# Optimization experiments

Measured on AMD Instinct MI355X. Metric: run time of the kernel, lower is better.

## Reference

```python
import jax, jax.numpy as jnp
import numpy as np

B, C, H, W = 2, 512, 48, 48
HEADS = 8
REDUCTION = 4
DPH = max(C // REDUCTION // HEADS, 1)   # 16
TOTAL = DPH * HEADS                      # 128
EPS_NORM = 1e-12
EPS_BN = 1e-5


def setup_inputs() -> dict:
    key = jax.random.key(0)
    ks = jax.random.split(key, 6)
    x = jax.random.normal(ks[0], (B, C, H, W), dtype=jnp.float32)
    # 1x1 convs stored as [out_ch, in_ch] matrices
    w_qkv = jax.random.normal(ks[1], (3 * TOTAL, C), dtype=jnp.float32) * (1.0 / np.sqrt(C))
    w_out = jax.random.normal(ks[2], (C, TOTAL), dtype=jnp.float32) * (1.0 / np.sqrt(TOTAL))
    temperature = jnp.ones((HEADS, 1, 1), dtype=jnp.float32)
    bn_gamma = jnp.ones((C,), dtype=jnp.float32)
    bn_beta = jnp.zeros((C,), dtype=jnp.float32)
    return {"x": x, "w_qkv": w_qkv, "temperature": temperature,
            "w_out": w_out, "bn_gamma": bn_gamma, "bn_beta": bn_beta}


def _l2norm(t):
    # F.normalize(t, dim=-1): t / max(||t||_2, eps)
    n = jnp.sqrt(jnp.sum(t * t, axis=-1, keepdims=True))
    return t / jnp.maximum(n, EPS_NORM)


def reference(x, w_qkv, temperature, w_out, bn_gamma, bn_beta):
    b, c, h, w = x.shape
    n = h * w
    # qkv 1x1 conv: [b, 3*TOTAL, h, w]
    qkv = jnp.einsum('bchw,oc->bohw', x, w_qkv)
    q, k, v = jnp.split(qkv, 3, axis=1)
    # [b, heads, dph, n] -> [b, heads, n, dph]
    def heads_tokens(t):
        return t.reshape(b, HEADS, DPH, n).transpose(0, 1, 3, 2)
    q = _l2norm(heads_tokens(q))
    k = _l2norm(heads_tokens(k))
    v = heads_tokens(v)
    # [b, heads, n, n]
    attn = jnp.einsum('bhnd,bhmd->bhnm', q, k) * temperature[None]
    attn = jax.nn.softmax(attn, axis=-1)
    out = jnp.einsum('bhnm,bhmd->bhnd', attn, v)          # [b, heads, n, dph]
    out = out.transpose(0, 1, 3, 2).reshape(b, TOTAL, h, w)
    # project_out: 1x1 conv then BatchNorm2d (training-mode batch stats)
    out = jnp.einsum('bthw,ct->bchw', out, w_out)
    mean = jnp.mean(out, axis=(0, 2, 3))
    var = jnp.mean((out - mean[None, :, None, None]) ** 2, axis=(0, 2, 3))
    out = (out - mean[None, :, None, None]) * jax.lax.rsqrt(var + EPS_BN)[None, :, None, None]
    out = out * bn_gamma[None, :, None, None] + bn_beta[None, :, None, None]
    return out
```

## Files before the change

### kernel.cpp

```cpp
#include <hip/hip_runtime.h>

#define NB 2
#define CC 512
#define NN 2304
#define NH 8
#define DD 16
#define TT 128
#define O3 384

typedef __attribute__((ext_vector_type(4))) float f32x4;
typedef __attribute__((ext_vector_type(8))) __bf16 bf16x8;
typedef __attribute__((ext_vector_type(4))) __bf16 bf16x4;
typedef __attribute__((ext_vector_type(4))) _Float16 f16x4;
typedef __attribute__((ext_vector_type(2))) __fp16 hf16x2;

union hf2pair {
    hf16x2 h[2];
    f16x4  v;
};

#define OFF_Q  0u
#define OFF_K  1179648u
#define OFF_VT 2359296u
#define OFF_AO 3538944u

__global__ __launch_bounds__(256) void k1_qkv(
    const float* __restrict__ x, const float* __restrict__ wqkv,
    _Float16* __restrict__ Q, _Float16* __restrict__ K, _Float16* __restrict__ VT)
{
    __shared__ __bf16 As[64][520];
    int ob = blockIdx.x, nt = blockIdx.y, b = blockIdx.z;
    int tid = threadIdx.x;
    int lane = tid & 63, wave = tid >> 6;
    int quad = lane >> 4, col = lane & 15;
    int n0 = nt * 64;
    int o0 = ob * 64;

    {
        int cb = tid >> 4;
        int nq = (tid & 15) * 4;
#pragma unroll
        for (int it = 0; it < 32; ++it) {
            int c = it * 16 + cb;
            f32x4 v = *(const f32x4*)(x + ((size_t)b * CC + c) * NN + n0 + nq);
            As[nq + 0][c] = (__bf16)v[0];
            As[nq + 1][c] = (__bf16)v[1];
            As[nq + 2][c] = (__bf16)v[2];
            As[nq + 3][c] = (__bf16)v[3];
        }
    }
    __syncthreads();

    f32x4 acc0 = {0.f,0.f,0.f,0.f}, acc1 = {0.f,0.f,0.f,0.f};
    f32x4 acc2 = {0.f,0.f,0.f,0.f}, acc3 = {0.f,0.f,0.f,0.f};

    int nrow = wave * 16 + col;
    const float* w0p = wqkv + (size_t)(o0 + col) * CC + quad * 8;
    const float* w1p = w0p + 16 * CC;
    const float* w2p = w0p + 32 * CC;
    const float* w3p = w0p + 48 * CC;

    f32x4 cw0a = *(const f32x4*)(w0p),     cw0b = *(const f32x4*)(w0p + 4);
    f32x4 cw1a = *(const f32x4*)(w1p),     cw1b = *(const f32x4*)(w1p + 4);
    f32x4 cw2a = *(const f32x4*)(w2p),     cw2b = *(const f32x4*)(w2p + 4);
    f32x4 cw3a = *(const f32x4*)(w3p),     cw3b = *(const f32x4*)(w3p + 4);

#pragma unroll
    for (int ks = 0; ks < 16; ks++) {
        f32x4 nw0a, nw0b, nw1a, nw1b, nw2a, nw2b, nw3a, nw3b;
        if (ks < 15) {
            nw0a = *(const f32x4*)(w0p + (ks + 1) * 32);
            nw0b = *(const f32x4*)(w0p + (ks + 1) * 32 + 4);
            nw1a = *(const f32x4*)(w1p + (ks + 1) * 32);
            nw1b = *(const f32x4*)(w1p + (ks + 1) * 32 + 4);
            nw2a = *(const f32x4*)(w2p + (ks + 1) * 32);
            nw2b = *(const f32x4*)(w2p + (ks + 1) * 32 + 4);
            nw3a = *(const f32x4*)(w3p + (ks + 1) * 32);
            nw3b = *(const f32x4*)(w3p + (ks + 1) * 32 + 4);
        }
        bf16x8 a = *(const bf16x8*)(&As[nrow][quad * 8 + ks * 32]);
        bf16x8 wf0, wf1, wf2, wf3;
#pragma unroll
        for (int j = 0; j < 4; j++) {
            wf0[j] = (__bf16)cw0a[j]; wf0[j + 4] = (__bf16)cw0b[j];
            wf1[j] = (__bf16)cw1a[j]; wf1[j + 4] = (__bf16)cw1b[j];
            wf2[j] = (__bf16)cw2a[j]; wf2[j + 4] = (__bf16)cw2b[j];
            wf3[j] = (__bf16)cw3a[j]; wf3[j + 4] = (__bf16)cw3b[j];
        }
        acc0 = __builtin_amdgcn_mfma_f32_16x16x32_bf16(a, wf0, acc0, 0, 0, 0);
        acc1 = __builtin_amdgcn_mfma_f32_16x16x32_bf16(a, wf1, acc1, 0, 0, 0);
        acc2 = __builtin_amdgcn_mfma_f32_16x16x32_bf16(a, wf2, acc2, 0, 0, 0);
        acc3 = __builtin_amdgcn_mfma_f32_16x16x32_bf16(a, wf3, acc3, 0, 0, 0);
        cw0a = nw0a; cw0b = nw0b; cw1a = nw1a; cw1b = nw1b;
        cw2a = nw2a; cw2b = nw2b; cw3a = nw3a; cw3b = nw3b;
    }

#pragma unroll
    for (int s = 0; s < 4; s++) {
        int oc = o0 + s * 16 + col;
        int d = oc & 15, h = (oc >> 4) & 7, kind = oc >> 7;
        f32x4 v = (s == 0) ? acc0 : (s == 1) ? acc1 : (s == 2) ? acc2 : acc3;
        if (kind < 2) {
            float ss0 = v[0] * v[0], ss1 = v[1] * v[1], ss2 = v[2] * v[2], ss3 = v[3] * v[3];
#pragma unroll
            for (int m = 1; m < 16; m <<= 1) {
                ss0 += __shfl_xor(ss0, m);
                ss1 += __shfl_xor(ss1, m);
                ss2 += __shfl_xor(ss2, m);
                ss3 += __shfl_xor(ss3, m);
            }
            v[0] *= 1.0f / fmaxf(sqrtf(ss0), 1e-12f);
            v[1] *= 1.0f / fmaxf(sqrtf(ss1), 1e-12f);
            v[2] *= 1.0f / fmaxf(sqrtf(ss2), 1e-12f);
            v[3] *= 1.0f / fmaxf(sqrtf(ss3), 1e-12f);
            _Float16* dst = (kind == 0 ? Q : K) + (size_t)(b * NH + h) * NN * DD;
#pragma unroll
            for (int r = 0; r < 4; r++) {
                int n = n0 + wave * 16 + quad * 4 + r;
                dst[(size_t)n * DD + d] = (_Float16)v[r];
            }
        } else {
            f16x4 pk;
#pragma unroll
            for (int r = 0; r < 4; r++) pk[r] = (_Float16)v[r];
            int n = n0 + wave * 16 + quad * 4;
            *(f16x4*)(VT + (size_t)((b * NH + h) * DD + d) * NN + n) = pk;
        }
    }
}

__global__ __launch_bounds__(512) void k2_attn(
    const _Float16* __restrict__ Q, const _Float16* __restrict__ K,
    const _Float16* __restrict__ VT, const float* __restrict__ temp,
    __bf16* __restrict__ AO)
{
    __shared__ float Osh[8][16][64];
    __shared__ float Lsh[8][64];

    int qt = blockIdx.x, bh = blockIdx.y;
    int lane = threadIdx.x & 63, wave = threadIdx.x >> 6;
    int quad = lane >> 4, col = lane & 15;
    int kbase = wave * 288;
    int qbase = qt * 64;

    const _Float16* Qb = Q + (size_t)bh * NN * DD;
    float tl2 = temp[bh & 7] * 1.4426950408889634f;
    _Float16 tl2h = (_Float16)tl2;

    f16x4 qf0 = *(const f16x4*)(Qb + (size_t)(qbase +  0 + col) * DD + quad * 4);
    f16x4 qf1 = *(const f16x4*)(Qb + (size_t)(qbase + 16 + col) * DD + quad * 4);
    f16x4 qf2 = *(const f16x4*)(Qb + (size_t)(qbase + 32 + col) * DD + quad * 4);
    f16x4 qf3 = *(const f16x4*)(Qb + (size_t)(qbase + 48 + col) * DD + quad * 4);
#pragma unroll
    for (int j = 0; j < 4; j++) {
        qf0[j] *= tl2h; qf1[j] *= tl2h; qf2[j] *= tl2h; qf3[j] *= tl2h;
    }
    const f16x4 onesf = {(_Float16)1.f, (_Float16)1.f, (_Float16)1.f, (_Float16)1.f};

    f32x4 oa0 = {0.f,0.f,0.f,0.f}, oa1 = {0.f,0.f,0.f,0.f};
    f32x4 oa2 = {0.f,0.f,0.f,0.f}, oa3 = {0.f,0.f,0.f,0.f};
    f32x4 lc0 = {0.f,0.f,0.f,0.f}, lc1 = {0.f,0.f,0.f,0.f};
    f32x4 lc2 = {0.f,0.f,0.f,0.f}, lc3 = {0.f,0.f,0.f,0.f};
    const f32x4 zc = {0.f,0.f,0.f,0.f};

    const _Float16* kp = K + (size_t)bh * NN * DD + (size_t)(kbase + col) * DD + quad * 4;
    const _Float16* vp = VT + (size_t)bh * DD * NN + (size_t)col * NN + kbase + quad * 4;

    f16x4 kfa = *(const f16x4*)(kp);
    f16x4 kfb = *(const f16x4*)(kp + 16 * DD);
    f16x4 vfa = *(const f16x4*)(vp);
    f16x4 vfb = *(const f16x4*)(vp + 16);

#define K2_CHUNK(KF, VF)                                                        \
    {                                                                           \
        f32x4 s0 = __builtin_amdgcn_mfma_f32_16x16x16f16(KF, qf0, zc, 0, 0, 0); \
        f32x4 s1 = __builtin_amdgcn_mfma_f32_16x16x16f16(KF, qf1, zc, 0, 0, 0); \
        f32x4 s2 = __builtin_amdgcn_mfma_f32_16x16x16f16(KF, qf2, zc, 0, 0, 0); \
        f32x4 s3 = __builtin_amdgcn_mfma_f32_16x16x16f16(KF, qf3, zc, 0, 0, 0); \
        hf2pair u0, u1, u2, u3;                                                 \
        u0.h[0] = __builtin_amdgcn_cvt_pkrtz(__builtin_amdgcn_exp2f(s0[0]),     \
                                             __builtin_amdgcn_exp2f(s0[1]));    \
        u0.h[1] = __builtin_amdgcn_cvt_pkrtz(__builtin_amdgcn_exp2f(s0[2]),     \
                                             __builtin_amdgcn_exp2f(s0[3]));    \
        u1.h[0] = __builtin_amdgcn_cvt_pkrtz(__builtin_amdgcn_exp2f(s1[0]),     \
                                             __builtin_amdgcn_exp2f(s1[1]));    \
        u1.h[1] = __builtin_amdgcn_cvt_pkrtz(__builtin_amdgcn_exp2f(s1[2]),     \
                                             __builtin_amdgcn_exp2f(s1[3]));    \
        u2.h[0] = __builtin_amdgcn_cvt_pkrtz(__builtin_amdgcn_exp2f(s2[0]),     \
                                             __builtin_amdgcn_exp2f(s2[1]));    \
        u2.h[1] = __builtin_amdgcn_cvt_pkrtz(__builtin_amdgcn_exp2f(s2[2]),     \
                                             __builtin_amdgcn_exp2f(s2[3]));    \
        u3.h[0] = __builtin_amdgcn_cvt_pkrtz(__builtin_amdgcn_exp2f(s3[0]),     \
                                             __builtin_amdgcn_exp2f(s3[1]));    \
        u3.h[1] = __builtin_amdgcn_cvt_pkrtz(__builtin_amdgcn_exp2f(s3[2]),     \
                                             __builtin_amdgcn_exp2f(s3[3]));    \
        f16x4 p0 = u0.v, p1 = u1.v, p2 = u2.v, p3 = u3.v;                       \
        lc0 = __builtin_amdgcn_mfma_f32_16x16x16f16(onesf, p0, lc0, 0, 0, 0);   \
        lc1 = __builtin_amdgcn_mfma_f32_16x16x16f16(onesf, p1, lc1, 0, 0, 0);   \
        lc2 = __builtin_amdgcn_mfma_f32_16x16x16f16(onesf, p2, lc2, 0, 0, 0);   \
        lc3 = __builtin_amdgcn_mfma_f32_16x16x16f16(onesf, p3, lc3, 0, 0, 0);   \
        oa0 = __builtin_amdgcn_mfma_f32_16x16x16f16(VF, p0, oa0, 0, 0, 0);      \
        oa1 = __builtin_amdgcn_mfma_f32_16x16x16f16(VF, p1, oa1, 0, 0, 0);      \
        oa2 = __builtin_amdgcn_mfma_f32_16x16x16f16(VF, p2, oa2, 0, 0, 0);      \
        oa3 = __builtin_amdgcn_mfma_f32_16x16x16f16(VF, p3, oa3, 0, 0, 0);      \
    }

    for (int g = 0; g < 9; ++g) {
        f16x4 kna, knb, vna, vnb;
        if (g < 8) {
            kna = *(const f16x4*)(kp + 32 * DD);
            knb = *(const f16x4*)(kp + 48 * DD);
            vna = *(const f16x4*)(vp + 32);
            vnb = *(const f16x4*)(vp + 48);
        }
        K2_CHUNK(kfa, vfa)
        K2_CHUNK(kfb, vfb)
        kfa = kna; kfb = knb; vfa = vna; vfb = vnb;
        kp += 32 * DD; vp += 32;
    }
#undef K2_CHUNK

#pragma unroll
    for (int r = 0; r < 4; ++r) {
        Osh[wave][quad * 4 + r][ 0 + col] = oa0[r];
        Osh[wave][quad * 4 + r][16 + col] = oa1[r];
        Osh[wave][quad * 4 + r][32 + col] = oa2[r];
        Osh[wave][quad * 4 + r][48 + col] = oa3[r];
    }
    float lv = (quad == 0) ? lc0[0] : (quad == 1) ? lc1[0] : (quad == 2) ? lc2[0] : lc3[0];
    Lsh[wave][quad * 16 + col] = lv;
    __syncthreads();

    int t = threadIdx.x;
    int q = t & 63, dg = t >> 6;
    float l = 0.f;
#pragma unroll
    for (int w = 0; w < 8; ++w) l += Lsh[w][q];
    float inv = 1.0f / l;
    float o0 = 0.f, o1 = 0.f;
#pragma unroll
    for (int w = 0; w < 8; ++w) {
        o0 += Osh[w][dg * 2 + 0][q];
        o1 += Osh[w][dg * 2 + 1][q];
    }
    int b = bh >> 3, h = bh & 7;
    __bf16* dst = AO + (size_t)(b * NN + qbase + q) * TT + h * DD + dg * 2;
    dst[0] = (__bf16)(o0 * inv);
    dst[1] = (__bf16)(o1 * inv);
}

__global__ __launch_bounds__(256) void k3_proj(
    const __bf16* __restrict__ AO, const float* __restrict__ wout,
    float* __restrict__ out)
{
    int cb = blockIdx.x, nt = blockIdx.y, b = blockIdx.z;
    int lane = threadIdx.x & 63, wave = threadIdx.x >> 6;
    int quad = lane >> 4, col = lane & 15;
    int n0 = nt * 64 + wave * 16, c0 = cb * 32;

    f32x4 acc0 = {0.f, 0.f, 0.f, 0.f};
    f32x4 acc1 = {0.f, 0.f, 0.f, 0.f};

    const __bf16* ab  = AO + (size_t)(b * NN + n0 + col) * TT + quad * 8;
    const float*  wb0 = wout + (size_t)(c0 + col) * TT + quad * 8;
    const float*  wb1 = wb0 + 16 * TT;
#pragma unroll
    for (int ks = 0; ks < 4; ks++) {
        bf16x8 a = *(const bf16x8*)(ab + ks * 32);
        f32x4 wA = *(const f32x4*)(wb0 + ks * 32);
        f32x4 wB = *(const f32x4*)(wb0 + ks * 32 + 4);
        f32x4 wC = *(const f32x4*)(wb1 + ks * 32);
        f32x4 wD = *(const f32x4*)(wb1 + ks * 32 + 4);
        bf16x8 w0, w1;
#pragma unroll
        for (int j = 0; j < 4; j++) {
            w0[j]     = (__bf16)wA[j];
            w0[j + 4] = (__bf16)wB[j];
            w1[j]     = (__bf16)wC[j];
            w1[j + 4] = (__bf16)wD[j];
        }
        acc0 = __builtin_amdgcn_mfma_f32_16x16x32_bf16(a, w0, acc0, 0, 0, 0);
        acc1 = __builtin_amdgcn_mfma_f32_16x16x32_bf16(a, w1, acc1, 0, 0, 0);
    }
#pragma unroll
    for (int s = 0; s < 2; s++) {
        int c = c0 + s * 16 + col;
        float* dst = out + (size_t)(b * CC + c) * NN + n0 + quad * 4;
        *(f32x4*)dst = (s == 0) ? acc0 : acc1;
    }
}

__global__ __launch_bounds__(256) void k4_bn(
    float* __restrict__ out, const float* __restrict__ gamma,
    const float* __restrict__ beta)
{
    int c = blockIdx.x;
    int t = threadIdx.x;
    float vals[18];
    float s = 0.f, q = 0.f;
#pragma unroll
    for (int i = 0; i < 18; i++) {
        int j = i * 256 + t;
        int b = j / NN, n = j % NN;
        float v = out[(size_t)(b * CC + c) * NN + n];
        vals[i] = v; s += v; q += v * v;
    }
#pragma unroll
    for (int m = 1; m < 64; m <<= 1) { s += __shfl_xor(s, m); q += __shfl_xor(q, m); }
    __shared__ float rs[4], rq[4];
    int lane = t & 63, wave = t >> 6;
    if (lane == 0) { rs[wave] = s; rq[wave] = q; }
    __syncthreads();
    s = rs[0] + rs[1] + rs[2] + rs[3];
    q = rq[0] + rq[1] + rq[2] + rq[3];
    float mean = s * (1.0f / 4608.0f);
    float var = q * (1.0f / 4608.0f) - mean * mean;
    float sc = rsqrtf(var + 1e-5f) * gamma[c];
    float sh = beta[c] - mean * sc;
#pragma unroll
    for (int i = 0; i < 18; i++) {
        int j = i * 256 + t;
        int b = j / NN, n = j % NN;
        out[(size_t)(b * CC + c) * NN + n] = vals[i] * sc + sh;
    }
}

extern "C" void kernel_launch(void* const* d_in, const int* in_sizes, int n_in,
                              void* d_out, int out_size, void* d_ws, size_t ws_size,
                              hipStream_t stream) {
    const float* x     = (const float*)d_in[0];
    const float* wqkv  = (const float*)d_in[1];
    const float* temp  = (const float*)d_in[2];
    const float* wout  = (const float*)d_in[3];
    const float* gamma = (const float*)d_in[4];
    const float* beta  = (const float*)d_in[5];
    float* out = (float*)d_out;
    char* ws = (char*)d_ws;

    _Float16* Q  = (_Float16*)(ws + OFF_Q);
    _Float16* K  = (_Float16*)(ws + OFF_K);
    _Float16* VT = (_Float16*)(ws + OFF_VT);
    __bf16*   AO = (__bf16*)(ws + OFF_AO);

    k1_qkv<<<dim3(6, 36, 2), 256, 0, stream>>>(x, wqkv, Q, K, VT);
    k2_attn<<<dim3(36, 16), 512, 0, stream>>>(Q, K, VT, temp, AO);
    k3_proj<<<dim3(16, 36, 2), 256, 0, stream>>>(AO, wout, out);
    k4_bn<<<512, 256, 0, stream>>>(out, gamma, beta);
}
```

Measured before the change: 148.5 us.

## Pre-convert weights to bf16 and compute all QKV outputs per x tile

Adds a small kernel that converts both weight matrices to bf16 in workspace, so the GEMM kernels load bf16 weights directly instead of converting fp32 on the fly. The QKV kernel now uses 512 threads per block, and each block computes all 384 output channels for one 64-token tile. The x tile is staged into shared memory once rather than six times across output-channel blocks. The cost is an extra launch and only 72 blocks in k1, which lowers parallelism and raises register pressure with 12 accumulators per wave.

```diff
diff --git a/kernel.cpp b/kernel.cpp
--- a/kernel.cpp
+++ b/kernel.cpp
@@ -19,29 +19,43 @@
     f16x4  v;
 };
 
-#define OFF_Q  0u
-#define OFF_K  1179648u
-#define OFF_VT 2359296u
-#define OFF_AO 3538944u
-
-__global__ __launch_bounds__(256) void k1_qkv(
-    const float* __restrict__ x, const float* __restrict__ wqkv,
+#define OFF_WQ 0u
+#define OFF_WO 393216u
+#define OFF_Q  524288u
+#define OFF_K  1703936u
+#define OFF_VT 2883584u
+#define OFF_AO 4063232u
+
+__global__ __launch_bounds__(256) void k0w(
+    const float* __restrict__ wqkv, const float* __restrict__ wout,
+    __bf16* __restrict__ wqb, __bf16* __restrict__ wob)
+{
+    int base = blockIdx.x * 4096 + threadIdx.x;
+#pragma unroll
+    for (int i = 0; i < 16; i++) {
+        int j = base + i * 256;
+        if (j < O3 * CC) wqb[j] = (__bf16)wqkv[j];
+        else             wob[j - O3 * CC] = (__bf16)wout[j - O3 * CC];
+    }
+}
+
+__global__ __launch_bounds__(512) void k1_qkv(
+    const float* __restrict__ x, const __bf16* __restrict__ wqb,
     _Float16* __restrict__ Q, _Float16* __restrict__ K, _Float16* __restrict__ VT)
 {
     __shared__ __bf16 As[64][520];
-    int ob = blockIdx.x, nt = blockIdx.y, b = blockIdx.z;
+    int nt = blockIdx.x, b = blockIdx.y;
     int tid = threadIdx.x;
     int lane = tid & 63, wave = tid >> 6;
     int quad = lane >> 4, col = lane & 15;
     int n0 = nt * 64;
-    int o0 = ob * 64;
 
     {
-        int cb = tid >> 4;
         int nq = (tid & 15) * 4;
-#pragma unroll
-        for (int it = 0; it < 32; ++it) {
-            int c = it * 16 + cb;
+        int cs = tid >> 4;
+#pragma unroll
+        for (int it = 0; it < 16; ++it) {
+            int c = it * 32 + cs;
             f32x4 v = *(const f32x4*)(x + ((size_t)b * CC + c) * NN + n0 + nq);
             As[nq + 0][c] = (__bf16)v[0];
             As[nq + 1][c] = (__bf16)v[1];
@@ -51,55 +65,31 @@
     }
     __syncthreads();
 
-    f32x4 acc0 = {0.f,0.f,0.f,0.f}, acc1 = {0.f,0.f,0.f,0.f};
-    f32x4 acc2 = {0.f,0.f,0.f,0.f}, acc3 = {0.f,0.f,0.f,0.f};
-
-    int nrow = wave * 16 + col;
-    const float* w0p = wqkv + (size_t)(o0 + col) * CC + quad * 8;
-    const float* w1p = w0p + 16 * CC;
-    const float* w2p = w0p + 32 * CC;
-    const float* w3p = w0p + 48 * CC;
-
-    f32x4 cw0a = *(const f32x4*)(w0p),     cw0b = *(const f32x4*)(w0p + 4);
-    f32x4 cw1a = *(const f32x4*)(w1p),     cw1b = *(const f32x4*)(w1p + 4);
-    f32x4 cw2a = *(const f32x4*)(w2p),     cw2b = *(const f32x4*)(w2p + 4);
-    f32x4 cw3a = *(const f32x4*)(w3p),     cw3b = *(const f32x4*)(w3p + 4);
+    int ng = wave & 3;
+    int og = wave >> 2;
+    int nrow = ng * 16 + col;
+
+    f32x4 acc[12];
+#pragma unroll
+    for (int s = 0; s < 12; s++) acc[s] = (f32x4){0.f, 0.f, 0.f, 0.f};
+
+    const __bf16* wbase = wqb + (size_t)(og * 192 + col) * CC + quad * 8;
 
 #pragma unroll
     for (int ks = 0; ks < 16; ks++) {
-        f32x4 nw0a, nw0b, nw1a, nw1b, nw2a, nw2b, nw3a, nw3b;
-        if (ks < 15) {
-            nw0a = *(const f32x4*)(w0p + (ks + 1) * 32);
-            nw0b = *(const f32x4*)(w0p + (ks + 1) * 32 + 4);
-            nw1a = *(const f32x4*)(w1p + (ks + 1) * 32);
-            nw1b = *(const f32x4*)(w1p + (ks + 1) * 32 + 4);
-            nw2a = *(const f32x4*)(w2p + (ks + 1) * 32);
-            nw2b = *(const f32x4*)(w2p + (ks + 1) * 32 + 4);
-            nw3a = *(const f32x4*)(w3p + (ks + 1) * 32);
-            nw3b = *(const f32x4*)(w3p + (ks + 1) * 32 + 4);
+        bf16x8 a = *(const bf16x8*)(&As[nrow][quad * 8 + ks * 32]);
+#pragma unroll
+        for (int s = 0; s < 12; s++) {
+            bf16x8 w = *(const bf16x8*)(wbase + (size_t)(s * 16) * CC + ks * 32);
+            acc[s] = __builtin_amdgcn_mfma_f32_16x16x32_bf16(a, w, acc[s], 0, 0, 0);
         }
-        bf16x8 a = *(const bf16x8*)(&As[nrow][quad * 8 + ks * 32]);
-        bf16x8 wf0, wf1, wf2, wf3;
-#pragma unroll
-        for (int j = 0; j < 4; j++) {
-            wf0[j] = (__bf16)cw0a[j]; wf0[j + 4] = (__bf16)cw0b[j];
-            wf1[j] = (__bf16)cw1a[j]; wf1[j + 4] = (__bf16)cw1b[j];
-            wf2[j] = (__bf16)cw2a[j]; wf2[j + 4] = (__bf16)cw2b[j];
-            wf3[j] = (__bf16)cw3a[j]; wf3[j + 4] = (__bf16)cw3b[j];
-        }
-        acc0 = __builtin_amdgcn_mfma_f32_16x16x32_bf16(a, wf0, acc0, 0, 0, 0);
-        acc1 = __builtin_amdgcn_mfma_f32_16x16x32_bf16(a, wf1, acc1, 0, 0, 0);
-        acc2 = __builtin_amdgcn_mfma_f32_16x16x32_bf16(a, wf2, acc2, 0, 0, 0);
-        acc3 = __builtin_amdgcn_mfma_f32_16x16x32_bf16(a, wf3, acc3, 0, 0, 0);
-        cw0a = nw0a; cw0b = nw0b; cw1a = nw1a; cw1b = nw1b;
-        cw2a = nw2a; cw2b = nw2b; cw3a = nw3a; cw3b = nw3b;
-    }
-
-#pragma unroll
-    for (int s = 0; s < 4; s++) {
-        int oc = o0 + s * 16 + col;
+    }
+
+#pragma unroll
+    for (int s = 0; s < 12; s++) {
+        int oc = og * 192 + s * 16 + col;
         int d = oc & 15, h = (oc >> 4) & 7, kind = oc >> 7;
-        f32x4 v = (s == 0) ? acc0 : (s == 1) ? acc1 : (s == 2) ? acc2 : acc3;
+        f32x4 v = acc[s];
         if (kind < 2) {
             float ss0 = v[0] * v[0], ss1 = v[1] * v[1], ss2 = v[2] * v[2], ss3 = v[3] * v[3];
 #pragma unroll
@@ -116,14 +106,14 @@
             _Float16* dst = (kind == 0 ? Q : K) + (size_t)(b * NH + h) * NN * DD;
 #pragma unroll
             for (int r = 0; r < 4; r++) {
-                int n = n0 + wave * 16 + quad * 4 + r;
+                int n = n0 + ng * 16 + quad * 4 + r;
                 dst[(size_t)n * DD + d] = (_Float16)v[r];
             }
         } else {
             f16x4 pk;
 #pragma unroll
             for (int r = 0; r < 4; r++) pk[r] = (_Float16)v[r];
-            int n = n0 + wave * 16 + quad * 4;
+            int n = n0 + ng * 16 + quad * 4;
             *(f16x4*)(VT + (size_t)((b * NH + h) * DD + d) * NN + n) = pk;
         }
     }
@@ -250,7 +240,7 @@
 }
 
 __global__ __launch_bounds__(256) void k3_proj(
-    const __bf16* __restrict__ AO, const float* __restrict__ wout,
+    const __bf16* __restrict__ AO, const __bf16* __restrict__ wob,
     float* __restrict__ out)
 {
     int cb = blockIdx.x, nt = blockIdx.y, b = blockIdx.z;
@@ -261,24 +251,14 @@
     f32x4 acc0 = {0.f, 0.f, 0.f, 0.f};
     f32x4 acc1 = {0.f, 0.f, 0.f, 0.f};
 
-    const __bf16* ab  = AO + (size_t)(b * NN + n0 + col) * TT + quad * 8;
-    const float*  wb0 = wout + (size_t)(c0 + col) * TT + quad * 8;
-    const float*  wb1 = wb0 + 16 * TT;
+    const __bf16* ab = AO + (size_t)(b * NN + n0 + col) * TT + quad * 8;
+    const __bf16* wb0 = wob + (size_t)(c0 + col) * TT + quad * 8;
+    const __bf16* wb1 = wb0 + 16 * TT;
 #pragma unroll
     for (int ks = 0; ks < 4; ks++) {
-        bf16x8 a = *(const bf16x8*)(ab + ks * 32);
-        f32x4 wA = *(const f32x4*)(wb0 + ks * 32);
-        f32x4 wB = *(const f32x4*)(wb0 + ks * 32 + 4);
-        f32x4 wC = *(const f32x4*)(wb1 + ks * 32);
-        f32x4 wD = *(const f32x4*)(wb1 + ks * 32 + 4);
-        bf16x8 w0, w1;
-#pragma unroll
-        for (int j = 0; j < 4; j++) {
-            w0[j]     = (__bf16)wA[j];
-            w0[j + 4] = (__bf16)wB[j];
-            w1[j]     = (__bf16)wC[j];
-            w1[j + 4] = (__bf16)wD[j];
-        }
+        bf16x8 a  = *(const bf16x8*)(ab + ks * 32);
+        bf16x8 w0 = *(const bf16x8*)(wb0 + ks * 32);
+        bf16x8 w1 = *(const bf16x8*)(wb1 + ks * 32);
         acc0 = __builtin_amdgcn_mfma_f32_16x16x32_bf16(a, w0, acc0, 0, 0, 0);
         acc1 = __builtin_amdgcn_mfma_f32_16x16x32_bf16(a, w1, acc1, 0, 0, 0);
     }
@@ -337,13 +317,16 @@
     float* out = (float*)d_out;
     char* ws = (char*)d_ws;
 
-    _Float16* Q  = (_Float16*)(ws + OFF_Q);
-    _Float16* K  = (_Float16*)(ws + OFF_K);
-    _Float16* VT = (_Float16*)(ws + OFF_VT);
-    __bf16*   AO = (__bf16*)(ws + OFF_AO);
-
-    k1_qkv<<<dim3(6, 36, 2), 256, 0, stream>>>(x, wqkv, Q, K, VT);
+    __bf16*   wqb = (__bf16*)(ws + OFF_WQ);
+    __bf16*   wob = (__bf16*)(ws + OFF_WO);
+    _Float16* Q   = (_Float16*)(ws + OFF_Q);
+    _Float16* K   = (_Float16*)(ws + OFF_K);
+    _Float16* VT  = (_Float16*)(ws + OFF_VT);
+    __bf16*   AO  = (__bf16*)(ws + OFF_AO);
+
+    k0w<<<64, 256, 0, stream>>>(wqkv, wout, wqb, wob);
+    k1_qkv<<<dim3(36, 2), 512, 0, stream>>>(x, wqb, Q, K, VT);
     k2_attn<<<dim3(36, 16), 512, 0, stream>>>(Q, K, VT, temp, AO);
-    k3_proj<<<dim3(16, 36, 2), 256, 0, stream>>>(AO, wout, out);
+    k3_proj<<<dim3(16, 36, 2), 256, 0, stream>>>(AO, wob, out);
     k4_bn<<<512, 256, 0, stream>>>(out, gamma, beta);
 }
```

Measured after the change: 174.5 us. 1.17x slower.
